# Kernel tuning notes

Hardware: AMD Instinct MI355X
Metric: run time of the kernel (lower is better)

Reference implementation:

```python
import jax, jax.numpy as jnp
import numpy as np

B, T, L, D, H = 4, 8, 197, 512, 8
DK = D // H
SIM_TH = 0.0
N = T * (L - 1)  # 1568 local tokens

def _ln(x, g, b, eps=1e-5):
    x32 = x.astype(jnp.float32)
    m = jnp.mean(x32, axis=-1, keepdims=True)
    v = jnp.mean((x32 - m) ** 2, axis=-1, keepdims=True)
    return (((x32 - m) * jax.lax.rsqrt(v + eps)) * g + b).astype(x.dtype)

def _qgelu(x):
    return x * jax.nn.sigmoid(1.702 * x)

def _mha(x, w_in, b_in, w_out, b_out):
    # torch nn.MultiheadAttention, x: [S, Bt, D] (seq-first)
    S, Bt, _ = x.shape
    qkv = x @ w_in.T + b_in
    q, k, v = jnp.split(qkv, 3, axis=-1)
    q = q.reshape(S, Bt, H, DK); k = k.reshape(S, Bt, H, DK); v = v.reshape(S, Bt, H, DK)
    scores = jnp.einsum('sbhd,tbhd->bhst', q, k) / jnp.sqrt(jnp.asarray(DK, x.dtype))
    p = jax.nn.softmax(scores, axis=-1)
    o = jnp.einsum('bhst,tbhd->sbhd', p, v).reshape(S, Bt, D)
    return o @ w_out.T + b_out

def _resblock(x, ln1g, ln1b, inw, inb, outw, outb, ln2g, ln2b, fcw, fcb, pw, pb):
    x = x + _mha(_ln(x, ln1g, ln1b), inw, inb, outw, outb)
    h = _qgelu(_ln(x, ln2g, ln2b) @ fcw.T + fcb)
    return x + h @ pw.T + pb

def _build_graph(x, g_mask):
    xd = jax.lax.stop_gradient(x)  # matches x.detach()
    xn = xd / jnp.maximum(jnp.linalg.norm(xd, axis=-1, keepdims=True), 1e-12)
    sim = jnp.einsum('bnd,bmd->bnm', xn, xn)
    adj = jnp.where(sim < SIM_TH, 0.0, sim)
    return adj * g_mask  # t != 1 branch

def _graph_attn(x, mask, wq, bq, wk, bk, wv, bv, wo, bo):
    Bb, Nn, _ = x.shape
    def heads(a):
        return a.reshape(Bb, Nn, H, DK).transpose(0, 2, 1, 3)
    Q = heads(x @ wq.T + bq); K = heads(x @ wk.T + bk); V = heads(x @ wv.T + bv)
    scores = jnp.einsum('bhnd,bhmd->bhnm', Q, K) / jnp.sqrt(jnp.asarray(DK, x.dtype))
    m = mask[:, None]  # [b,1,N,N]
    scores = jnp.where(m == 0, -jnp.inf, scores * m)  # scores*mask then masked_fill(mask==0,-inf)
    p = jax.nn.softmax(scores, axis=-1)
    o = jnp.einsum('bhnm,bhmd->bhnd', p, V).transpose(0, 2, 1, 3).reshape(Bb, Nn, D)
    return o @ wo.T + bo

def _forward(x, proj_w, proj_b,
             m_ln1g, m_ln1b, m_inw, m_inb, m_outw, m_outb,
             m_ln2g, m_ln2b, m_fcw, m_fcb, m_pw, m_pb,
             g_wq, g_bq, g_wk, g_bk, g_wv, g_bv, g_wo, g_bo,
             ln1g, ln1b, a_inw, a_inb, a_outw, a_outb,
             ln2g, ln2b, fcw, fcb, pw, pb, g_mask):
    b, t, l, d = x.shape
    x = x @ proj_w.T + proj_b
    glob = x[:, :, 0, :].transpose(1, 0, 2)  # [t,b,d]
    msg = (m_ln1g, m_ln1b, m_inw, m_inb, m_outw, m_outb, m_ln2g, m_ln2b, m_fcw, m_fcb, m_pw, m_pb)
    glob = _resblock(glob, *msg)
    glob = _resblock(glob, *msg)  # message_attn applied twice (shared weights)
    glob = glob.reshape(1, t, b, d)
    loc = x[:, :, 1:, :].reshape(b, t * (l - 1), d)
    gm = _build_graph(loc, g_mask)
    loc = _graph_attn(loc, gm, g_wq, g_bq, g_wk, g_bk, g_wv, g_bv, g_wo, g_bo)
    loc = loc.reshape(b, t, l - 1, d).transpose(2, 1, 0, 3)  # [l-1,t,b,d]
    y = jnp.concatenate([glob, loc], axis=0).reshape(l, t * b, d)
    y = y + _mha(_ln(y, ln1g, ln1b), a_inw, a_inb, a_outw, a_outb)
    y = y + _qgelu(_ln(y, ln2g, ln2b) @ fcw.T + fcb) @ pw.T + pb
    return y.reshape(l, t, b, d).transpose(2, 1, 0, 3)  # [b,t,l,d]

def setup_inputs() -> dict:
    key = jax.random.key(0)
    ks = jax.random.split(key, 64)
    s = 0.02
    def w(i, shape):
        return jax.random.normal(ks[i], shape, jnp.float32) * s
    ones = jnp.ones((D,), jnp.float32); zeros = jnp.zeros((D,), jnp.float32)
    gm = (jax.random.uniform(ks[60], (N, N)) < 0.5).astype(jnp.float32)
    gm = gm.at[jnp.arange(N), jnp.arange(N)].set(1.0)  # keep self-edges so no row is fully masked
    return dict(
        x=jax.random.normal(ks[0], (B, T, L, D), jnp.float32),
        proj_w=w(1, (D, D)), proj_b=jnp.zeros((D,), jnp.float32),
        m_ln1g=ones, m_ln1b=zeros,
        m_inw=w(2, (3 * D, D)), m_inb=jnp.zeros((3 * D,), jnp.float32),
        m_outw=w(3, (D, D)), m_outb=zeros,
        m_ln2g=ones, m_ln2b=zeros,
        m_fcw=w(4, (4 * D, D)), m_fcb=jnp.zeros((4 * D,), jnp.float32),
        m_pw=w(5, (D, 4 * D)), m_pb=zeros,
        g_wq=w(6, (D, D)), g_bq=zeros, g_wk=w(7, (D, D)), g_bk=zeros,
        g_wv=w(8, (D, D)), g_bv=zeros, g_wo=w(9, (D, D)), g_bo=zeros,
        ln1g=ones, ln1b=zeros,
        a_inw=w(10, (3 * D, D)), a_inb=jnp.zeros((3 * D,), jnp.float32),
        a_outw=w(11, (D, D)), a_outb=zeros,
        ln2g=ones, ln2b=zeros,
        fcw=w(12, (4 * D, D)), fcb=jnp.zeros((4 * D,), jnp.float32),
        pw=w(13, (D, 4 * D)), pb=zeros,
        g_mask=gm,
    )

def reference(x, proj_w, proj_b, m_ln1g, m_ln1b, m_inw, m_inb, m_outw, m_outb,
              m_ln2g, m_ln2b, m_fcw, m_fcb, m_pw, m_pb,
              g_wq, g_bq, g_wk, g_bk, g_wv, g_bv, g_wo, g_bo,
              ln1g, ln1b, a_inw, a_inb, a_outw, a_outb,
              ln2g, ln2b, fcw, fcb, pw, pb, g_mask):
    return _forward(x, proj_w, proj_b, m_ln1g, m_ln1b, m_inw, m_inb, m_outw, m_outb,
                    m_ln2g, m_ln2b, m_fcw, m_fcb, m_pw, m_pb,
                    g_wq, g_bq, g_wk, g_bk, g_wv, g_bv, g_wo, g_bo,
                    ln1g, ln1b, a_inw, a_inb, a_outw, a_outb,
                    ln2g, ln2b, fcw, fcb, pw, pb, g_mask)
```

## Files before the change

kernel.cpp:

```cpp
#include <hip/hip_runtime.h>
#include <hip/hip_bf16.h>

typedef unsigned short u16;
typedef __attribute__((ext_vector_type(8))) short bf16x8;
typedef __attribute__((ext_vector_type(4))) float f32x4;

#define FINF __builtin_huge_valf()

static __device__ __forceinline__ float bf2f(u16 v){ union{unsigned u; float f;} c; c.u = ((unsigned)v)<<16; return c.f; }
static __device__ __forceinline__ u16 f2bf(float f){ union{__hip_bfloat16 h; u16 u;} c; c.h = __float2bfloat16(f); return c.u; }
static __device__ __forceinline__ bf16x8 scale8(bf16x8 v, float s){
  bf16x8 o;
  #pragma unroll
  for (int e=0;e<8;e++) o[e] = (short)f2bf(bf2f((u16)v[e])*s);
  return o;
}

static __device__ __forceinline__ void gload16(const void* g, void* l){
  __builtin_amdgcn_global_load_lds(
      (const __attribute__((address_space(1))) void*)g,
      (__attribute__((address_space(3))) void*)l, 16, 0, 0);
}

#define WAIT_VM0()   { asm volatile("s_waitcnt vmcnt(0)" ::: "memory"); __builtin_amdgcn_sched_barrier(0); }
#define BARRIER()    { __builtin_amdgcn_sched_barrier(0); __builtin_amdgcn_s_barrier(); __builtin_amdgcn_sched_barrier(0); }

struct CvtArgs {
  const float* src[14];
  u16* dst[14];
  int n[14];
};
__global__ __launch_bounds__(256) void cvt_multi(CvtArgs a){
  int seg = blockIdx.y;
  const float* s = a.src[seg]; u16* d = a.dst[seg]; int n = a.n[seg];
  for (int i = (blockIdx.x*256 + threadIdx.x)*4; i < n; i += gridDim.x*256*4){
    float4 v = *(const float4*)(s + i);
    ushort4 o = { f2bf(v.x), f2bf(v.y), f2bf(v.z), f2bf(v.w) };
    *(ushort4*)(d + i) = o;
  }
}

__global__ __launch_bounds__(256) void concat_bias(const float* a, const float* b, const float* c, float* o){
  int i = blockIdx.x*256 + threadIdx.x;
  o[i] = i < 512 ? a[i] : (i < 1024 ? b[i-512] : c[i-1024]);
}

template<int BM, int EPI, int MW>
__global__ __launch_bounds__(256,MW) void gemm_nt(
    const u16* __restrict__ A, const u16* __restrict__ Bw,
    const float* __restrict__ bias, const float* aux, void* out,
    int M, int Nn, int K, int ldc, long aBatch, long bBatch, long cBatch)
{
  constexpr int MI = BM/32;
  constexpr int WSPAN = BM/2;
  __shared__ __align__(16) u16 a_lds[2*BM*64];
  __shared__ __align__(16) u16 b_lds[2*128*64];
  const int z = blockIdx.z;
  const u16* Az = A + (long)z*aBatch;
  const u16* Bz = Bw + (long)z*bBatch;
  const int n0 = blockIdx.x*128, m0 = blockIdx.y*BM;
  const int t = threadIdx.x, lane = t & 63, wave = t >> 6;
  const int wr = wave >> 1, wc = wave & 1;
  const int r = lane & 15, kq = lane >> 4;

  const int srow = t >> 3;
  const int scol = ((t&7)*8) ^ ((srow&7)<<3);
  int rowA[MI], rowB[4];
  #pragma unroll
  for (int i=0;i<MI;i++){ int ga = m0 + i*32 + srow; rowA[i] = ga < M ? ga : M-1; }
  #pragma unroll
  for (int i=0;i<4;i++){ int gb = n0 + i*32 + srow; rowB[i] = gb < Nn ? gb : Nn-1; }

  f32x4 acc[MI][4] = {};
  const int nkt = K >> 6;

  auto STAGE = [&](int kt, int buf){
    const long koff = (long)kt*64 + scol;
    #pragma unroll
    for (int i=0;i<MI;i++)
      gload16(Az + (long)rowA[i]*K + koff, (char*)a_lds + buf*(BM*128) + i*4096 + wave*1024);
    #pragma unroll
    for (int i=0;i<4;i++)
      gload16(Bz + (long)rowB[i]*K + koff, (char*)b_lds + buf*16384 + i*4096 + wave*1024);
  };

  STAGE(0,0);
  WAIT_VM0(); BARRIER();
  for (int kt=0; kt<nkt; kt++){
    const int cur = kt&1;
    if (kt+1 < nkt) STAGE(kt+1, cur^1);
    const u16* al = a_lds + cur*BM*64;
    const u16* bl = b_lds + cur*8192;
    #pragma unroll
    for (int kk=0; kk<2; kk++){
      bf16x8 af[MI], bfr[4];
      #pragma unroll
      for (int i=0;i<MI;i++){
        int rw = wr*WSPAN + i*16 + r;
        af[i] = *(const bf16x8*)&al[rw*64 + ((kk*32 + kq*8) ^ ((rw&7)<<3))];
      }
      #pragma unroll
      for (int j=0;j<4;j++){
        int rw = wc*64 + j*16 + r;
        bfr[j] = *(const bf16x8*)&bl[rw*64 + ((kk*32 + kq*8) ^ ((rw&7)<<3))];
      }
      #pragma unroll
      for (int i=0;i<MI;i++)
        #pragma unroll
        for (int j=0;j<4;j++)
          acc[i][j] = __builtin_amdgcn_mfma_f32_16x16x32_bf16(af[i], bfr[j], acc[i][j], 0,0,0);
    }
    WAIT_VM0(); BARRIER();
  }

  #pragma unroll
  for (int i=0;i<MI;i++){
    #pragma unroll
    for (int j=0;j<4;j++){
      int gcol = n0 + wc*64 + j*16 + r;
      if (gcol >= Nn) continue;
      float bv = bias ? bias[gcol] : 0.f;
      #pragma unroll
      for (int rr=0; rr<4; rr++){
        int grow = m0 + wr*WSPAN + i*16 + kq*4 + rr;
        if (grow >= M) continue;
        float v = acc[i][j][rr] + bv;
        if constexpr (EPI==0){
          ((float*)out)[(long)z*cBatch + (long)grow*ldc + gcol] = v;
        } else if constexpr (EPI==1){
          ((u16*)out)[(long)z*cBatch + (long)grow*ldc + gcol] = f2bf(v);
        } else if constexpr (EPI==2){
          long idx = (long)z*cBatch + (long)grow*ldc + gcol;
          ((float*)out)[idx] = aux[idx] + v;
        } else if constexpr (EPI==3){
          float g = v / (1.f + __expf(-1.702f*v));
          ((u16*)out)[(long)z*cBatch + (long)grow*ldc + gcol] = f2bf(g);
        } else if constexpr (EPI==4){
          float adj = v < 0.f ? 0.f : v;
          float gmv = aux[(long)grow*Nn + gcol];
          ((u16*)out)[(long)z*cBatch + (long)grow*ldc + gcol] = f2bf(adj*gmv);
        } else if constexpr (EPI==5){
          int b = grow/1568, n = grow%1568, tt = n/196, lp = n%196;
          int yrow = (1+lp)*32 + tt*4 + b;
          ((float*)out)[(long)yrow*ldc + gcol] = v;
        } else if constexpr (EPI==6){
          long idx = (long)grow*ldc + gcol;
          int l = grow>>5, rb = grow&31, tt = rb>>2, bb = rb&3;
          ((float*)out)[((long)((bb*8+tt)*197) + l)*512 + gcol] = aux[idx] + v;
        }
      }
    }
  }
}

__global__ __launch_bounds__(256) void transpose_v(
    const u16* __restrict__ src, u16* __restrict__ vt,
    int nrows, long zofs, long nofs, int vcol0, int outld)
{
  __shared__ u16 tile[64][66];
  const int t = threadIdx.x;
  const int nt = blockIdx.x, h = blockIdx.y, z = blockIdx.z;
  const int n0 = nt*64;
  const int rlo = t>>3, c0 = (t&7)*8;
  #pragma unroll
  for (int i=0;i<2;i++){
    int nl = i*32 + rlo;
    int n = n0 + nl; int nc = n < nrows ? n : nrows-1;
    const u16* s = src + (long)z*zofs + (long)nc*nofs + vcol0 + h*64 + c0;
    uint4 v = *(const uint4*)s;
    bool dead = n >= nrows;
    #pragma unroll
    for (int e=0;e<8;e++) tile[nl][c0+e] = dead ? (u16)0 : ((const u16*)&v)[e];
  }
  __syncthreads();
  #pragma unroll
  for (int i=0;i<2;i++){
    int d = i*32 + rlo;
    u16 tmp[8];
    #pragma unroll
    for (int e=0;e<8;e++) tmp[e] = tile[c0+e][d];
    int ncol = n0 + c0;
    if (ncol + 8 <= outld){
      u16* dst = vt + ((long)((z*8+h)*64 + d))*outld + ncol;
      *(uint4*)dst = *(uint4*)tmp;
    }
  }
}

template<bool MASKED>
__global__ __launch_bounds__(256,4) void flash3(
    const u16* __restrict__ QKV, const u16* __restrict__ VT,
    const u16* __restrict__ gmask, u16* __restrict__ Out,
    int nq, int nk, int nqb, long qBatch, long qRow,
    long oBatch, long oRow, long gmBatch, int vtld)
{
  __shared__ __align__(16) u16 k_lds[2*4096];
  __shared__ __align__(16) u16 p_lds[4][1024];
  int h, z, qb;
  if constexpr (MASKED){
    int id = blockIdx.x;
    int a = id>>6, c = id&7; h = (id>>3)&7;
    int G = a*8 + c;
    if (G >= 4*nqb) return;
    z = G / nqb; qb = G % nqb;
  } else {
    qb = blockIdx.x; h = blockIdx.y; z = blockIdx.z;
  }
  const int t = threadIdx.x, lane = t&63, wave = t>>6;
  const int r = lane&15, kq = lane>>4;
  const u16* Qb = QKV + (long)z*qBatch + h*64;
  const u16* Kb = Qb + 512;
  const u16* Vt = VT + (long)(z*8+h)*64*vtld;
  const int qt0 = qb*64;
  const int q0  = qt0 + wave*16;
  const int q   = q0 + r;
  const int qc  = q < nq ? q : nq-1;
  const u16* Gq = MASKED ? (gmask + (long)z*gmBatch + (long)qc*nk) : nullptr;

  bf16x8 qf0, qf1;
  { const u16* qp = Qb + (long)qc*qRow + kq*8;
    qf0 = scale8(*(const bf16x8*)qp, 0.125f);
    qf1 = scale8(*(const bf16x8*)(qp+32), 0.125f); }

  const int srow = t>>3;
  const int scol = ((t&7)*8) ^ ((srow&7)<<3);

  auto stage_k = [&](int kt, int buf){
    #pragma unroll
    for (int i=0;i<2;i++){
      int j = kt*64 + i*32 + srow; if (j > nk-1) j = nk-1;
      gload16(Kb + (long)j*qRow + scol, (char*)k_lds + buf*8192 + i*4096 + wave*1024);
    }
  };

  bf16x8 ONES;
  #pragma unroll
  for (int e=0;e<8;e++) ONES[e] = (short)0x3F80;

  float m_ = -FINF;
  f32x4 o_[4] = {};  f32x4 l_ = {};

  const int nkt = (nk + 63) >> 6;
  stage_k(0,0);
  __syncthreads();
  for (int kt=0; kt<nkt; kt++){
    const int cur = kt&1;
    if (kt+1 < nkt) stage_k(kt+1, cur^1);

    uint4 vfr[2][4];
    #pragma unroll
    for (int c=0;c<2;c++)
      #pragma unroll
      for (int j=0;j<4;j++)
        vfr[c][j] = *(const uint4*)(Vt + (long)(j*16+r)*vtld + kt*64 + c*32 + kq*8);
    ushort4 gv[4];
    if constexpr (MASKED){
      #pragma unroll
      for (int sub=0;sub<4;sub++)
        gv[sub] = *(const ushort4*)(Gq + kt*64 + sub*16 + kq*4);
    }

    const u16* kl = k_lds + cur*4096;
    float p[4][4];
    #pragma unroll
    for (int sub=0; sub<4; sub++){
      int rw = sub*16 + r; int sw = (rw&7)<<3;
      bf16x8 kf0 = *(const bf16x8*)&kl[rw*64 + ((kq*8) ^ sw)];
      bf16x8 kf1 = *(const bf16x8*)&kl[rw*64 + ((32 + kq*8) ^ sw)];
      f32x4 sc = {};
      sc = __builtin_amdgcn_mfma_f32_16x16x32_bf16(kf0, qf0, sc, 0,0,0);
      sc = __builtin_amdgcn_mfma_f32_16x16x32_bf16(kf1, qf1, sc, 0,0,0);
      #pragma unroll
      for (int rr=0;rr<4;rr++){
        float sv = sc[rr];
        int key = kt*64 + sub*16 + kq*4 + rr;
        if constexpr (MASKED){
          u16 g = ((const u16*)&gv[sub])[rr];
          sv = (g == 0 || key >= nk) ? -FINF : sv * bf2f(g);
        } else {
          if (key >= nk) sv = -FINF;
        }
        p[sub][rr] = sv;
      }
    }

    float mx;
    { float a0 = fmaxf(fmaxf(p[0][0],p[0][1]), fmaxf(p[0][2],p[0][3]));
      float a1 = fmaxf(fmaxf(p[1][0],p[1][1]), fmaxf(p[1][2],p[1][3]));
      float a2 = fmaxf(fmaxf(p[2][0],p[2][1]), fmaxf(p[2][2],p[2][3]));
      float a3 = fmaxf(fmaxf(p[3][0],p[3][1]), fmaxf(p[3][2],p[3][3]));
      mx = fmaxf(fmaxf(a0,a1), fmaxf(a2,a3)); }
    mx = fmaxf(mx, __shfl_xor(mx, 16));
    mx = fmaxf(mx, __shfl_xor(mx, 32));
    float mnew = fmaxf(m_, mx);
    float fac = (m_ == -FINF) ? 0.f : __expf(m_ - mnew);
    #pragma unroll
    for (int j=0;j<4;j++){ o_[j][0]*=fac; o_[j][1]*=fac; o_[j][2]*=fac; o_[j][3]*=fac; }
    l_[0]*=fac; l_[1]*=fac; l_[2]*=fac; l_[3]*=fac;
    m_ = mnew;

    #pragma unroll
    for (int sub=0;sub<4;sub++){
      float e0 = (p[sub][0] == -FINF) ? 0.f : __expf(p[sub][0] - mnew);
      float e1 = (p[sub][1] == -FINF) ? 0.f : __expf(p[sub][1] - mnew);
      float e2 = (p[sub][2] == -FINF) ? 0.f : __expf(p[sub][2] - mnew);
      float e3 = (p[sub][3] == -FINF) ? 0.f : __expf(p[sub][3] - mnew);
      unsigned u0, u1;
      asm volatile("v_cvt_pk_bf16_f32 %0, %1, %2" : "=v"(u0) : "v"(e0), "v"(e1));
      asm volatile("v_cvt_pk_bf16_f32 %0, %1, %2" : "=v"(u1) : "v"(e2), "v"(e3));
      uint2 w; w.x = u0; w.y = u1;
      int idx = r*64 + ((sub*16 + kq*4) ^ ((r&7)<<3));
      *(uint2*)&p_lds[wave][idx] = w;
    }

    #pragma unroll
    for (int c=0;c<2;c++){
      bf16x8 pf = *(const bf16x8*)&p_lds[wave][r*64 + ((c*32 + kq*8) ^ ((r&7)<<3))];
      #pragma unroll
      for (int j=0;j<4;j++){
        bf16x8 vf = *(const bf16x8*)&vfr[c][j];
        o_[j] = __builtin_amdgcn_mfma_f32_16x16x32_bf16(vf, pf, o_[j], 0,0,0);
      }
      l_ = __builtin_amdgcn_mfma_f32_16x16x32_bf16(ONES, pf, l_, 0,0,0);
    }
    __syncthreads();
  }

  float inv = l_[0] > 0.f ? 1.f/l_[0] : 0.f;
  if (q < nq){
    #pragma unroll
    for (int j=0;j<4;j++){
      ushort4 ov = { f2bf(o_[j][0]*inv), f2bf(o_[j][1]*inv),
                     f2bf(o_[j][2]*inv), f2bf(o_[j][3]*inv) };
      *(ushort4*)(Out + (long)z*oBatch + (long)q*oRow + h*64 + j*16 + kq*4) = ov;
    }
  }
}

__global__ __launch_bounds__(256) void ln_rows(const float* __restrict__ in,
    const float* __restrict__ g, const float* __restrict__ b, u16* __restrict__ out, int rows)
{
  int wave = threadIdx.x >> 6, lane = threadIdx.x & 63;
  int row = blockIdx.x*4 + wave;
  if (row >= rows) return;
  const float4* x = (const float4*)(in + (long)row*512);
  float4 v0 = x[lane], v1 = x[lane+64];
  float s  = v0.x+v0.y+v0.z+v0.w + v1.x+v1.y+v1.z+v1.w;
  float ss = v0.x*v0.x+v0.y*v0.y+v0.z*v0.z+v0.w*v0.w + v1.x*v1.x+v1.y*v1.y+v1.z*v1.z+v1.w*v1.w;
  #pragma unroll
  for (int d=1; d<64; d<<=1){ s += __shfl_xor(s,d); ss += __shfl_xor(ss,d); }
  float mean = s * (1.f/512.f);
  float var = ss * (1.f/512.f) - mean*mean;
  float rs = rsqrtf(var + 1e-5f);
  const float4* gg = (const float4*)g; const float4* bb = (const float4*)b;
  float4 g0 = gg[lane], g1 = gg[lane+64], b0 = bb[lane], b1 = bb[lane+64];
  u16* o = out + (long)row*512;
  ushort4 o0 = { f2bf((v0.x-mean)*rs*g0.x + b0.x), f2bf((v0.y-mean)*rs*g0.y + b0.y),
                 f2bf((v0.z-mean)*rs*g0.z + b0.z), f2bf((v0.w-mean)*rs*g0.w + b0.w) };
  ushort4 o1 = { f2bf((v1.x-mean)*rs*g1.x + b1.x), f2bf((v1.y-mean)*rs*g1.y + b1.y),
                 f2bf((v1.z-mean)*rs*g1.z + b1.z), f2bf((v1.w-mean)*rs*g1.w + b1.w) };
  *(ushort4*)(o + lane*4) = o0;
  *(ushort4*)(o + 256 + lane*4) = o1;
}

__global__ __launch_bounds__(256) void locprep(const float* __restrict__ y0,
    u16* __restrict__ xn, u16* __restrict__ locb)
{
  int wave = threadIdx.x >> 6, lane = threadIdx.x & 63;
  int rr = blockIdx.x*4 + wave;
  int bb = rr/1568, n = rr%1568, tt = n/196, lp = n%196;
  const float4* x = (const float4*)(y0 + ((long)((bb*8+tt)*197) + 1 + lp)*512);
  float4 v0 = x[lane], v1 = x[lane+64];
  float ss = v0.x*v0.x+v0.y*v0.y+v0.z*v0.z+v0.w*v0.w + v1.x*v1.x+v1.y*v1.y+v1.z*v1.z+v1.w*v1.w;
  #pragma unroll
  for (int d=1; d<64; d<<=1) ss += __shfl_xor(ss,d);
  float sc = 1.f / fmaxf(sqrtf(ss), 1e-12f);
  u16* ox = xn + (long)rr*512;
  u16* ol = locb + (long)rr*512;
  ushort4 a0 = { f2bf(v0.x*sc), f2bf(v0.y*sc), f2bf(v0.z*sc), f2bf(v0.w*sc) };
  ushort4 a1 = { f2bf(v1.x*sc), f2bf(v1.y*sc), f2bf(v1.z*sc), f2bf(v1.w*sc) };
  ushort4 c0 = { f2bf(v0.x), f2bf(v0.y), f2bf(v0.z), f2bf(v0.w) };
  ushort4 c1 = { f2bf(v1.x), f2bf(v1.y), f2bf(v1.z), f2bf(v1.w) };
  *(ushort4*)(ox + lane*4) = a0;  *(ushort4*)(ox + 256 + lane*4) = a1;
  *(ushort4*)(ol + lane*4) = c0;  *(ushort4*)(ol + 256 + lane*4) = c1;
}

__global__ __launch_bounds__(64) void msg_attn(const u16* __restrict__ mqkv, u16* __restrict__ matt){
  __shared__ float q_s[8][64], k_s[8][64], v_s[8][64];
  int bh = blockIdx.x; int bt = bh>>3, h = bh&7;
  int lane = threadIdx.x;
  int row = lane>>3, cc = (lane&7)*8;
  #pragma unroll
  for (int e=0;e<8;e++){
    long base = (long)(row*4 + bt)*1536 + h*64 + cc + e;
    q_s[row][cc+e] = bf2f(mqkv[base]);
    k_s[row][cc+e] = bf2f(mqkv[base + 512]);
    v_s[row][cc+e] = bf2f(mqkv[base + 1024]);
  }
  __syncthreads();
  int q = lane>>3, k = lane&7;
  float s = 0.f;
  #pragma unroll 16
  for (int d=0; d<64; d++) s += q_s[q][d]*k_s[k][d];
  s *= 0.125f;
  float mx = s;
  #pragma unroll
  for (int d=1; d<8; d<<=1) mx = fmaxf(mx, __shfl_xor(mx,d));
  float p = __expf(s - mx), ps = p;
  #pragma unroll
  for (int d=1; d<8; d<<=1) ps += __shfl_xor(ps,d);
  p /= ps;
  for (int d=0; d<64; d++){
    float ov = p * v_s[k][d];
    #pragma unroll
    for (int m=1; m<8; m<<=1) ov += __shfl_xor(ov,m);
    if (k == (d>>3)) matt[(long)(q*4 + bt)*512 + h*64 + d] = f2bf(ov);
  }
}

__global__ __launch_bounds__(256) void gather_glob(const float* __restrict__ y0, float* __restrict__ glob){
  int idx = blockIdx.x*256 + threadIdx.x;
  int orow = idx>>9, d = idx&511;
  int tt = orow>>2, bb = orow&3;
  glob[idx] = y0[((long)(bb*8+tt)*197)*512 + d];
}
__global__ __launch_bounds__(256) void copy32(const float* __restrict__ glob, float* __restrict__ y){
  int idx = blockIdx.x*256 + threadIdx.x;
  y[idx] = glob[idx];
}

extern "C" void kernel_launch(void* const* d_in, const int* in_sizes, int n_in,
                              void* d_out, int out_size, void* d_ws, size_t ws_size,
                              hipStream_t stream)
{
  const float* x      = (const float*)d_in[0];
  const float* proj_w = (const float*)d_in[1];
  const float* proj_b = (const float*)d_in[2];
  const float* m_ln1g = (const float*)d_in[3];
  const float* m_ln1b = (const float*)d_in[4];
  const float* m_inw  = (const float*)d_in[5];
  const float* m_inb  = (const float*)d_in[6];
  const float* m_outw = (const float*)d_in[7];
  const float* m_outb = (const float*)d_in[8];
  const float* m_ln2g = (const float*)d_in[9];
  const float* m_ln2b = (const float*)d_in[10];
  const float* m_fcw  = (const float*)d_in[11];
  const float* m_fcb  = (const float*)d_in[12];
  const float* m_pw   = (const float*)d_in[13];
  const float* m_pb   = (const float*)d_in[14];
  const float* g_wq = (const float*)d_in[15]; const float* g_bq = (const float*)d_in[16];
  const float* g_wk = (const float*)d_in[17]; const float* g_bk = (const float*)d_in[18];
  const float* g_wv = (const float*)d_in[19]; const float* g_bv = (const float*)d_in[20];
  const float* g_wo = (const float*)d_in[21]; const float* g_bo = (const float*)d_in[22];
  const float* ln1g = (const float*)d_in[23]; const float* ln1b = (const float*)d_in[24];
  const float* a_inw = (const float*)d_in[25]; const float* a_inb = (const float*)d_in[26];
  const float* a_outw = (const float*)d_in[27]; const float* a_outb = (const float*)d_in[28];
  const float* ln2g = (const float*)d_in[29]; const float* ln2b = (const float*)d_in[30];
  const float* fcw = (const float*)d_in[31]; const float* fcb = (const float*)d_in[32];
  const float* pw = (const float*)d_in[33]; const float* pb = (const float*)d_in[34];
  const float* g_mask = (const float*)d_in[35];

  if (ws_size < (size_t)99753984) return;

  char* ws = (char*)d_ws;
  u16* WB = (u16*)ws;
  const long WPROJ=0, WMIN=262144, WMOUT=1048576, WMFC=1310720, WMP=2359296,
             WGQ=3407872, WGK=3670016, WGV=3932160, WGO=4194304,
             WAIN=4456448, WAOUT=5242880, WFC=5505024, WP=6553600;
  float* y0   = (float*)(ws + 15204352);
  float* y    = (float*)(ws + 28114944);
  u16* lnbuf  = (u16*)(ws + 41025536);
  u16* vtg    = (u16*)(ws + 41025536);
  u16* locb   = (u16*)(ws + 47480832);
  u16* qkv    = (u16*)(ws + 53903360);
  u16* xb     = (u16*)(ws + 73269248);
  u16* gm     = (u16*)(ws + 73269248);
  u16* vt2    = (u16*)(ws + 73269248);
  u16* hbuf   = (u16*)(ws + 73269248);
  u16* obuf   = (u16*)(ws + 92938240);
  float* glob = (float*)(ws + 99393536);
  u16* mlnb   = (u16*)(ws + 99459072);
  u16* mqkv   = (u16*)(ws + 99491840);
  u16* matt   = (u16*)(ws + 99590144);
  u16* mh     = (u16*)(ws + 99622912);
  float* gbias = (float*)(ws + 99622912);

  CvtArgs ca;
  auto setseg=[&](int i, const float* s, u16* d, int n){ ca.src[i]=s; ca.dst[i]=d; ca.n[i]=n; };
  setseg(0,  x,      xb,       6304*512);
  setseg(1,  proj_w, WB+WPROJ, 262144);
  setseg(2,  m_inw,  WB+WMIN,  786432);
  setseg(3,  m_outw, WB+WMOUT, 262144);
  setseg(4,  m_fcw,  WB+WMFC,  1048576);
  setseg(5,  m_pw,   WB+WMP,   1048576);
  setseg(6,  g_wq,   WB+WGQ,   262144);
  setseg(7,  g_wk,   WB+WGK,   262144);
  setseg(8,  g_wv,   WB+WGV,   262144);
  setseg(9,  g_wo,   WB+WGO,   262144);
  setseg(10, a_inw,  WB+WAIN,  786432);
  setseg(11, a_outw, WB+WAOUT, 262144);
  setseg(12, fcw,    WB+WFC,   1048576);
  setseg(13, pw,     WB+WP,    1048576);
  cvt_multi<<<dim3(128,14), 256, 0, stream>>>(ca);

  gemm_nt<64,0,3><<<dim3(4,99), 256, 0, stream>>>(xb, WB+WPROJ, proj_b, nullptr, y0, 6304,512,512,512, 0,0,0);

  gather_glob<<<64,256,0,stream>>>(y0, glob);

  for (int it=0; it<2; ++it){
    ln_rows<<<8,256,0,stream>>>(glob, m_ln1g, m_ln1b, mlnb, 32);
    gemm_nt<64,1,3><<<dim3(12,1),256,0,stream>>>(mlnb, WB+WMIN, m_inb, nullptr, mqkv, 32,1536,512,1536, 0,0,0);
    msg_attn<<<32,64,0,stream>>>(mqkv, matt);
    gemm_nt<64,2,3><<<dim3(4,1),256,0,stream>>>(matt, WB+WMOUT, m_outb, glob, glob, 32,512,512,512, 0,0,0);
    ln_rows<<<8,256,0,stream>>>(glob, m_ln2g, m_ln2b, mlnb, 32);
    gemm_nt<64,3,3><<<dim3(16,1),256,0,stream>>>(mlnb, WB+WMFC, m_fcb, nullptr, mh, 32,2048,512,2048, 0,0,0);
    gemm_nt<64,2,3><<<dim3(4,1),256,0,stream>>>(mh, WB+WMP, m_pb, glob, glob, 32,512,2048,512, 0,0,0);
  }

  concat_bias<<<6,256,0,stream>>>(g_bq, g_bk, g_bv, gbias);

  locprep<<<1568,256,0,stream>>>(y0, lnbuf, locb);

  gemm_nt<64,4,3><<<dim3(13,25,4),256,0,stream>>>(lnbuf, lnbuf, nullptr, g_mask, gm,
      1568,1568,512,1568, 1568L*512, 1568L*512, 1568L*1568);

  gemm_nt<64,1,3><<<dim3(12,98),256,0,stream>>>(locb, WB+WGQ, gbias, nullptr, qkv, 6272,1536,512,1536, 0,0,0);

  transpose_v<<<dim3(25,8,4),256,0,stream>>>(qkv, vtg, 1568, 1568L*1536, 1536L, 1024, 1568);

  flash3<true><<<832,256,0,stream>>>(qkv, vtg, gm, obuf,
      1568,1568,25, 1568L*1536, 1536, 1568L*512, 512, 1568L*1568, 1568);

  gemm_nt<64,5,3><<<dim3(4,98),256,0,stream>>>(obuf, WB+WGO, g_bo, nullptr, y, 6272,512,512,512, 0,0,0);

  copy32<<<64,256,0,stream>>>(glob, y);

  ln_rows<<<1576,256,0,stream>>>(y, ln1g, ln1b, lnbuf, 6304);
  gemm_nt<64,1,3><<<dim3(12,99),256,0,stream>>>(lnbuf, WB+WAIN, a_inb, nullptr, qkv, 6304,1536,512,1536, 0,0,0);
  transpose_v<<<dim3(4,8,32),256,0,stream>>>(qkv, vt2, 197, 1536L, 32L*1536, 1024, 256);
  flash3<false><<<dim3(4,8,32),256,0,stream>>>(qkv, vt2, nullptr, obuf,
      197,197,4, 1536, 32L*1536, 512, 32L*512, 0, 256);
  gemm_nt<64,2,3><<<dim3(4,99),256,0,stream>>>(obuf, WB+WAOUT, a_outb, y, y, 6304,512,512,512, 0,0,0);

  ln_rows<<<1576,256,0,stream>>>(y, ln2g, ln2b, lnbuf, 6304);
  gemm_nt<64,3,3><<<dim3(16,99),256,0,stream>>>(lnbuf, WB+WFC, fcb, nullptr, hbuf, 6304,2048,512,2048, 0,0,0);
  gemm_nt<64,6,3><<<dim3(4,99),256,0,stream>>>(hbuf, WB+WP, pb, y, (float*)d_out, 6304,512,2048,512, 0,0,0);
}
```

Baseline: 569.5 us.

## Process two query tiles per flash block and shrink GEMM row tiles

```diff
diff --git a/kernel.cpp b/kernel.cpp
--- a/kernel.cpp
+++ b/kernel.cpp
@@ -188,14 +188,14 @@
 }
 
 template<bool MASKED>
-__global__ __launch_bounds__(256,4) void flash3(
+__global__ __launch_bounds__(256,3) void flash4(
     const u16* __restrict__ QKV, const u16* __restrict__ VT,
     const u16* __restrict__ gmask, u16* __restrict__ Out,
     int nq, int nk, int nqb, long qBatch, long qRow,
     long oBatch, long oRow, long gmBatch, int vtld)
 {
   __shared__ __align__(16) u16 k_lds[2*4096];
-  __shared__ __align__(16) u16 p_lds[4][1024];
+  __shared__ __align__(16) u16 p_lds[4][2][1024];
   int h, z, qb;
   if constexpr (MASKED){
     int id = blockIdx.x;
@@ -211,16 +211,20 @@
   const u16* Qb = QKV + (long)z*qBatch + h*64;
   const u16* Kb = Qb + 512;
   const u16* Vt = VT + (long)(z*8+h)*64*vtld;
-  const int qt0 = qb*64;
-  const int q0  = qt0 + wave*16;
-  const int q   = q0 + r;
-  const int qc  = q < nq ? q : nq-1;
-  const u16* Gq = MASKED ? (gmask + (long)z*gmBatch + (long)qc*nk) : nullptr;
-
-  bf16x8 qf0, qf1;
-  { const u16* qp = Qb + (long)qc*qRow + kq*8;
-    qf0 = scale8(*(const bf16x8*)qp, 0.125f);
-    qf1 = scale8(*(const bf16x8*)(qp+32), 0.125f); }
+  const int qt0 = qb*128;
+
+  int qi[2], qc[2];
+  bf16x8 qf[2][2];
+  const u16* Gq[2];
+  #pragma unroll
+  for (int qt=0; qt<2; qt++){
+    qi[qt] = qt0 + qt*64 + wave*16 + r;
+    qc[qt] = qi[qt] < nq ? qi[qt] : nq-1;
+    const u16* qp = Qb + (long)qc[qt]*qRow + kq*8;
+    qf[qt][0] = scale8(*(const bf16x8*)qp, 0.125f);
+    qf[qt][1] = scale8(*(const bf16x8*)(qp+32), 0.125f);
+    Gq[qt] = MASKED ? (gmask + (long)z*gmBatch + (long)qc[qt]*nk) : nullptr;
+  }
 
   const int srow = t>>3;
   const int scol = ((t&7)*8) ^ ((srow&7)<<3);
@@ -237,8 +241,8 @@
   #pragma unroll
   for (int e=0;e<8;e++) ONES[e] = (short)0x3F80;
 
-  float m_ = -FINF;
-  f32x4 o_[4] = {};  f32x4 l_ = {};
+  float m_[2] = {-FINF,-FINF};
+  f32x4 o_[2][4] = {};  f32x4 l_[2] = {};
 
   const int nkt = (nk + 63) >> 6;
   stage_k(0,0);
@@ -253,86 +257,96 @@
       #pragma unroll
       for (int j=0;j<4;j++)
         vfr[c][j] = *(const uint4*)(Vt + (long)(j*16+r)*vtld + kt*64 + c*32 + kq*8);
-    ushort4 gv[4];
-    if constexpr (MASKED){
-      #pragma unroll
-      for (int sub=0;sub<4;sub++)
-        gv[sub] = *(const ushort4*)(Gq + kt*64 + sub*16 + kq*4);
-    }
 
     const u16* kl = k_lds + cur*4096;
-    float p[4][4];
-    #pragma unroll
-    for (int sub=0; sub<4; sub++){
-      int rw = sub*16 + r; int sw = (rw&7)<<3;
-      bf16x8 kf0 = *(const bf16x8*)&kl[rw*64 + ((kq*8) ^ sw)];
-      bf16x8 kf1 = *(const bf16x8*)&kl[rw*64 + ((32 + kq*8) ^ sw)];
-      f32x4 sc = {};
-      sc = __builtin_amdgcn_mfma_f32_16x16x32_bf16(kf0, qf0, sc, 0,0,0);
-      sc = __builtin_amdgcn_mfma_f32_16x16x32_bf16(kf1, qf1, sc, 0,0,0);
-      #pragma unroll
-      for (int rr=0;rr<4;rr++){
-        float sv = sc[rr];
-        int key = kt*64 + sub*16 + kq*4 + rr;
-        if constexpr (MASKED){
-          u16 g = ((const u16*)&gv[sub])[rr];
-          sv = (g == 0 || key >= nk) ? -FINF : sv * bf2f(g);
-        } else {
-          if (key >= nk) sv = -FINF;
+    #pragma unroll
+    for (int qt=0; qt<2; qt++){
+      ushort4 gv[4];
+      if constexpr (MASKED){
+        #pragma unroll
+        for (int sub=0;sub<4;sub++)
+          gv[sub] = *(const ushort4*)(Gq[qt] + kt*64 + sub*16 + kq*4);
+      }
+
+      float p[4][4];
+      #pragma unroll
+      for (int sub=0; sub<4; sub++){
+        int rw = sub*16 + r; int sw = (rw&7)<<3;
+        bf16x8 kf0 = *(const bf16x8*)&kl[rw*64 + ((kq*8) ^ sw)];
+        bf16x8 kf1 = *(const bf16x8*)&kl[rw*64 + ((32 + kq*8) ^ sw)];
+        f32x4 sc = {};
+        sc = __builtin_amdgcn_mfma_f32_16x16x32_bf16(kf0, qf[qt][0], sc, 0,0,0);
+        sc = __builtin_amdgcn_mfma_f32_16x16x32_bf16(kf1, qf[qt][1], sc, 0,0,0);
+        #pragma unroll
+        for (int rr=0;rr<4;rr++){
+          float sv = sc[rr];
+          int key = kt*64 + sub*16 + kq*4 + rr;
+          if constexpr (MASKED){
+            u16 g = ((const u16*)&gv[sub])[rr];
+            sv = (g == 0 || key >= nk) ? -FINF : sv * bf2f(g);
+          } else {
+            if (key >= nk) sv = -FINF;
+          }
+          p[sub][rr] = sv;
         }
-        p[sub][rr] = sv;
-      }
-    }
-
-    float mx;
-    { float a0 = fmaxf(fmaxf(p[0][0],p[0][1]), fmaxf(p[0][2],p[0][3]));
-      float a1 = fmaxf(fmaxf(p[1][0],p[1][1]), fmaxf(p[1][2],p[1][3]));
-      float a2 = fmaxf(fmaxf(p[2][0],p[2][1]), fmaxf(p[2][2],p[2][3]));
-      float a3 = fmaxf(fmaxf(p[3][0],p[3][1]), fmaxf(p[3][2],p[3][3]));
-      mx = fmaxf(fmaxf(a0,a1), fmaxf(a2,a3)); }
-    mx = fmaxf(mx, __shfl_xor(mx, 16));
-    mx = fmaxf(mx, __shfl_xor(mx, 32));
-    float mnew = fmaxf(m_, mx);
-    float fac = (m_ == -FINF) ? 0.f : __expf(m_ - mnew);
-    #pragma unroll
-    for (int j=0;j<4;j++){ o_[j][0]*=fac; o_[j][1]*=fac; o_[j][2]*=fac; o_[j][3]*=fac; }
-    l_[0]*=fac; l_[1]*=fac; l_[2]*=fac; l_[3]*=fac;
-    m_ = mnew;
-
-    #pragma unroll
-    for (int sub=0;sub<4;sub++){
-      float e0 = (p[sub][0] == -FINF) ? 0.f : __expf(p[sub][0] - mnew);
-      float e1 = (p[sub][1] == -FINF) ? 0.f : __expf(p[sub][1] - mnew);
-      float e2 = (p[sub][2] == -FINF) ? 0.f : __expf(p[sub][2] - mnew);
-      float e3 = (p[sub][3] == -FINF) ? 0.f : __expf(p[sub][3] - mnew);
-      unsigned u0, u1;
-      asm volatile("v_cvt_pk_bf16_f32 %0, %1, %2" : "=v"(u0) : "v"(e0), "v"(e1));
-      asm volatile("v_cvt_pk_bf16_f32 %0, %1, %2" : "=v"(u1) : "v"(e2), "v"(e3));
-      uint2 w; w.x = u0; w.y = u1;
-      int idx = r*64 + ((sub*16 + kq*4) ^ ((r&7)<<3));
-      *(uint2*)&p_lds[wave][idx] = w;
-    }
-
-    #pragma unroll
-    for (int c=0;c<2;c++){
-      bf16x8 pf = *(const bf16x8*)&p_lds[wave][r*64 + ((c*32 + kq*8) ^ ((r&7)<<3))];
-      #pragma unroll
-      for (int j=0;j<4;j++){
-        bf16x8 vf = *(const bf16x8*)&vfr[c][j];
-        o_[j] = __builtin_amdgcn_mfma_f32_16x16x32_bf16(vf, pf, o_[j], 0,0,0);
-      }
-      l_ = __builtin_amdgcn_mfma_f32_16x16x32_bf16(ONES, pf, l_, 0,0,0);
+      }
+
+      float mx;
+      { float a0 = fmaxf(fmaxf(p[0][0],p[0][1]), fmaxf(p[0][2],p[0][3]));
+        float a1 = fmaxf(fmaxf(p[1][0],p[1][1]), fmaxf(p[1][2],p[1][3]));
+        float a2 = fmaxf(fmaxf(p[2][0],p[2][1]), fmaxf(p[2][2],p[2][3]));
+        float a3 = fmaxf(fmaxf(p[3][0],p[3][1]), fmaxf(p[3][2],p[3][3]));
+        mx = fmaxf(fmaxf(a0,a1), fmaxf(a2,a3)); }
+      mx = fmaxf(mx, __shfl_xor(mx, 16));
+      mx = fmaxf(mx, __shfl_xor(mx, 32));
+      float mnew = fmaxf(m_[qt], mx);
+      if (__any(mnew > m_[qt])){
+        float fac = (m_[qt] == -FINF) ? 0.f : __expf(m_[qt] - mnew);
+        #pragma unroll
+        for (int j=0;j<4;j++){ o_[qt][j][0]*=fac; o_[qt][j][1]*=fac; o_[qt][j][2]*=fac; o_[qt][j][3]*=fac; }
+        l_[qt][0]*=fac; l_[qt][1]*=fac; l_[qt][2]*=fac; l_[qt][3]*=fac;
+        m_[qt] = mnew;
+      }
+      mnew = m_[qt];
+
+      #pragma unroll
+      for (int sub=0;sub<4;sub++){
+        float e0 = (p[sub][0] == -FINF) ? 0.f : __expf(p[sub][0] - mnew);
+        float e1 = (p[sub][1] == -FINF) ? 0.f : __expf(p[sub][1] - mnew);
+        float e2 = (p[sub][2] == -FINF) ? 0.f : __expf(p[sub][2] - mnew);
+        float e3 = (p[sub][3] == -FINF) ? 0.f : __expf(p[sub][3] - mnew);
+        unsigned u0, u1;
+        asm volatile("v_cvt_pk_bf16_f32 %0, %1, %2" : "=v"(u0) : "v"(e0), "v"(e1));
+        asm volatile("v_cvt_pk_bf16_f32 %0, %1, %2" : "=v"(u1) : "v"(e2), "v"(e3));
+        uint2 w; w.x = u0; w.y = u1;
+        int idx = r*64 + ((sub*16 + kq*4) ^ ((r&7)<<3));
+        *(uint2*)&p_lds[wave][qt][idx] = w;
+      }
+
+      #pragma unroll
+      for (int c=0;c<2;c++){
+        bf16x8 pf = *(const bf16x8*)&p_lds[wave][qt][r*64 + ((c*32 + kq*8) ^ ((r&7)<<3))];
+        #pragma unroll
+        for (int j=0;j<4;j++){
+          bf16x8 vf = *(const bf16x8*)&vfr[c][j];
+          o_[qt][j] = __builtin_amdgcn_mfma_f32_16x16x32_bf16(vf, pf, o_[qt][j], 0,0,0);
+        }
+        l_[qt] = __builtin_amdgcn_mfma_f32_16x16x32_bf16(ONES, pf, l_[qt], 0,0,0);
+      }
     }
     __syncthreads();
   }
 
-  float inv = l_[0] > 0.f ? 1.f/l_[0] : 0.f;
-  if (q < nq){
-    #pragma unroll
-    for (int j=0;j<4;j++){
-      ushort4 ov = { f2bf(o_[j][0]*inv), f2bf(o_[j][1]*inv),
-                     f2bf(o_[j][2]*inv), f2bf(o_[j][3]*inv) };
-      *(ushort4*)(Out + (long)z*oBatch + (long)q*oRow + h*64 + j*16 + kq*4) = ov;
+  #pragma unroll
+  for (int qt=0; qt<2; qt++){
+    float inv = l_[qt][0] > 0.f ? 1.f/l_[qt][0] : 0.f;
+    if (qi[qt] < nq){
+      #pragma unroll
+      for (int j=0;j<4;j++){
+        ushort4 ov = { f2bf(o_[qt][j][0]*inv), f2bf(o_[qt][j][1]*inv),
+                       f2bf(o_[qt][j][2]*inv), f2bf(o_[qt][j][3]*inv) };
+        *(ushort4*)(Out + (long)z*oBatch + (long)qi[qt]*oRow + h*64 + j*16 + kq*4) = ov;
+      }
     }
   }
 }
@@ -503,18 +517,18 @@
   setseg(13, pw,     WB+WP,    1048576);
   cvt_multi<<<dim3(128,14), 256, 0, stream>>>(ca);
 
-  gemm_nt<64,0,3><<<dim3(4,99), 256, 0, stream>>>(xb, WB+WPROJ, proj_b, nullptr, y0, 6304,512,512,512, 0,0,0);
+  gemm_nt<32,0,4><<<dim3(4,197), 256, 0, stream>>>(xb, WB+WPROJ, proj_b, nullptr, y0, 6304,512,512,512, 0,0,0);
 
   gather_glob<<<64,256,0,stream>>>(y0, glob);
 
   for (int it=0; it<2; ++it){
     ln_rows<<<8,256,0,stream>>>(glob, m_ln1g, m_ln1b, mlnb, 32);
-    gemm_nt<64,1,3><<<dim3(12,1),256,0,stream>>>(mlnb, WB+WMIN, m_inb, nullptr, mqkv, 32,1536,512,1536, 0,0,0);
+    gemm_nt<32,1,4><<<dim3(12,1),256,0,stream>>>(mlnb, WB+WMIN, m_inb, nullptr, mqkv, 32,1536,512,1536, 0,0,0);
     msg_attn<<<32,64,0,stream>>>(mqkv, matt);
-    gemm_nt<64,2,3><<<dim3(4,1),256,0,stream>>>(matt, WB+WMOUT, m_outb, glob, glob, 32,512,512,512, 0,0,0);
+    gemm_nt<32,2,4><<<dim3(4,1),256,0,stream>>>(matt, WB+WMOUT, m_outb, glob, glob, 32,512,512,512, 0,0,0);
     ln_rows<<<8,256,0,stream>>>(glob, m_ln2g, m_ln2b, mlnb, 32);
-    gemm_nt<64,3,3><<<dim3(16,1),256,0,stream>>>(mlnb, WB+WMFC, m_fcb, nullptr, mh, 32,2048,512,2048, 0,0,0);
-    gemm_nt<64,2,3><<<dim3(4,1),256,0,stream>>>(mh, WB+WMP, m_pb, glob, glob, 32,512,2048,512, 0,0,0);
+    gemm_nt<32,3,4><<<dim3(16,1),256,0,stream>>>(mlnb, WB+WMFC, m_fcb, nullptr, mh, 32,2048,512,2048, 0,0,0);
+    gemm_nt<32,2,4><<<dim3(4,1),256,0,stream>>>(mh, WB+WMP, m_pb, glob, glob, 32,512,2048,512, 0,0,0);
   }
 
   concat_bias<<<6,256,0,stream>>>(g_bq, g_bk, g_bv, gbias);
@@ -528,21 +542,21 @@
 
   transpose_v<<<dim3(25,8,4),256,0,stream>>>(qkv, vtg, 1568, 1568L*1536, 1536L, 1024, 1568);
 
-  flash3<true><<<832,256,0,stream>>>(qkv, vtg, gm, obuf,
-      1568,1568,25, 1568L*1536, 1536, 1568L*512, 512, 1568L*1568, 1568);
-
-  gemm_nt<64,5,3><<<dim3(4,98),256,0,stream>>>(obuf, WB+WGO, g_bo, nullptr, y, 6272,512,512,512, 0,0,0);
+  flash4<true><<<448,256,0,stream>>>(qkv, vtg, gm, obuf,
+      1568,1568,13, 1568L*1536, 1536, 1568L*512, 512, 1568L*1568, 1568);
+
+  gemm_nt<32,5,4><<<dim3(4,196),256,0,stream>>>(obuf, WB+WGO, g_bo, nullptr, y, 6272,512,512,512, 0,0,0);
 
   copy32<<<64,256,0,stream>>>(glob, y);
 
   ln_rows<<<1576,256,0,stream>>>(y, ln1g, ln1b, lnbuf, 6304);
   gemm_nt<64,1,3><<<dim3(12,99),256,0,stream>>>(lnbuf, WB+WAIN, a_inb, nullptr, qkv, 6304,1536,512,1536, 0,0,0);
   transpose_v<<<dim3(4,8,32),256,0,stream>>>(qkv, vt2, 197, 1536L, 32L*1536, 1024, 256);
-  flash3<false><<<dim3(4,8,32),256,0,stream>>>(qkv, vt2, nullptr, obuf,
-      197,197,4, 1536, 32L*1536, 512, 32L*512, 0, 256);
-  gemm_nt<64,2,3><<<dim3(4,99),256,0,stream>>>(obuf, WB+WAOUT, a_outb, y, y, 6304,512,512,512, 0,0,0);
+  flash4<false><<<dim3(2,8,32),256,0,stream>>>(qkv, vt2, nullptr, obuf,
+      197,197,2, 1536, 32L*1536, 512, 32L*512, 0, 256);
+  gemm_nt<32,2,4><<<dim3(4,197),256,0,stream>>>(obuf, WB+WAOUT, a_outb, y, y, 6304,512,512,512, 0,0,0);
 
   ln_rows<<<1576,256,0,stream>>>(y, ln2g, ln2b, lnbuf, 6304);
   gemm_nt<64,3,3><<<dim3(16,99),256,0,stream>>>(lnbuf, WB+WFC, fcb, nullptr, hbuf, 6304,2048,512,2048, 0,0,0);
-  gemm_nt<64,6,3><<<dim3(4,99),256,0,stream>>>(hbuf, WB+WP, pb, y, (float*)d_out, 6304,512,2048,512, 0,0,0);
-}
+  gemm_nt<32,6,4><<<dim3(4,197),256,0,stream>>>(hbuf, WB+WP, pb, y, (float*)d_out, 6304,512,2048,512, 0,0,0);
+}
```

Result: faster. 520.7 us, median of 3 (-8.6%).
